# Performance work log

Measured on AMD Instinct MI355X. Metric: run time of the kernel, lower is better.

## Reference

```python
import jax, jax.numpy as jnp
import numpy as np

EPS = 1e-6
NQ, NKV, D, HID = 40, 8, 128, 5120
QKV_DIM = (NQ + 2 * NKV) * D + NQ  # gating enabled


def rmsnorm(x, w):
    xf = x.astype(jnp.float32)
    n = jax.lax.rsqrt(jnp.mean(xf * xf, axis=-1, keepdims=True) + EPS)
    return (xf * n).astype(x.dtype) * w


def rope(x, cos, sin):
    # x: [B,S,h,d], cos/sin: [B,S,d]
    d = x.shape[-1]
    c = cos[..., None, :d]
    s = sin[..., None, :d]
    x1, x2 = x[..., : d // 2], x[..., d // 2 :]
    rot = jnp.concatenate([-x2, x1], axis=-1)
    return x * c + rot * s


def setup_inputs() -> dict:
    key = jax.random.key(0)
    ks = jax.random.split(key, 8)
    B, S = 1, 2048
    return {
        "x": jax.random.normal(ks[0], (B, S, HID), jnp.float32),
        "rope_cos": jax.random.normal(ks[1], (B, S, D), jnp.float32),
        "rope_sin": jax.random.normal(ks[2], (B, S, D), jnp.float32),
        "w_pre_norm": jnp.ones((HID,), jnp.float32),
        "w_qkv": jax.random.normal(ks[3], (HID, QKV_DIM), jnp.float32) * 0.02,
        "w_q_norm": jnp.ones((D,), jnp.float32),
        "w_k_norm": jnp.ones((D,), jnp.float32),
        "w_proj": jax.random.normal(ks[4], (NQ * D, HID), jnp.float32) * 0.02,
    }


def reference(x, rope_cos, rope_sin, w_pre_norm, w_qkv, w_q_norm, w_k_norm, w_proj):
    B, S, _ = x.shape
    normed = rmsnorm(x, w_pre_norm)
    qkv = normed @ w_qkv  # [B,S,QKV_DIM]
    q_dim, k_dim = NQ * D, NKV * D
    q = qkv[..., :q_dim].reshape(B, S, NQ, D)
    k = qkv[..., q_dim : q_dim + k_dim].reshape(B, S, NKV, D)
    v = qkv[..., q_dim + k_dim : q_dim + 2 * k_dim].reshape(B, S, NKV, D)
    gate = jax.nn.sigmoid(qkv[..., q_dim + 2 * k_dim :])  # [B,S,NQ]
    q = rmsnorm(q, w_q_norm)
    k = rmsnorm(k, w_k_norm)
    q = rope(q, rope_cos, rope_sin)
    k = rope(k, rope_cos, rope_sin)
    # GQA: expand kv groups to query heads
    rep = NQ // NKV
    k = jnp.repeat(k, rep, axis=2)  # [B,S,NQ,D]
    v = jnp.repeat(v, rep, axis=2)
    scale = 1.0 / jnp.sqrt(jnp.float32(D))
    scores = jnp.einsum("bqhd,bkhd->bhqk", q, k) * scale
    attn = jax.nn.softmax(scores, axis=-1)
    out = jnp.einsum("bhqk,bkhd->bqhd", attn, v)  # [B,S,NQ,D]
    out = out * gate[..., None]
    out = out.reshape(B, S, NQ * D)
    return out @ w_proj
```

## Files before the change

kernel.cpp:

```cpp
#include <hip/hip_runtime.h>
#include <hip/hip_bf16.h>
#include <stdint.h>

#define S_LEN 2048
#define NQh   40
#define NKVh  8
#define HD    128
#define HIDd  5120
#define QKV_C 7208
#define QKV_P 7424
#define NROW  (S_LEN * NQh)

typedef unsigned short u16;
typedef short bf16x8 __attribute__((ext_vector_type(8)));
typedef float f32x4  __attribute__((ext_vector_type(4)));
typedef u16   u16x4  __attribute__((ext_vector_type(4)));

typedef const __attribute__((address_space(1))) void* gas_ptr;
typedef __attribute__((address_space(3))) void*       las_ptr;

#define MFMA16(a, b, c) __builtin_amdgcn_mfma_f32_16x16x32_bf16(a, b, c, 0, 0, 0)

__device__ __forceinline__ u16 f2bf(float f) {
  union { float f; unsigned u; } v; v.f = f;
  return (u16)((v.u + 0x7fffu + ((v.u >> 16) & 1u)) >> 16);
}
__device__ __forceinline__ u16 f2bf_c(float f) {
  union { __hip_bfloat16 b; u16 u; } v;
  v.b = __float2bfloat16(f);
  return v.u;
}
__device__ __forceinline__ float b2f(u16 b) {
  union { unsigned u; float f; } v; v.u = ((unsigned)b) << 16; return v.f;
}

__device__ __forceinline__ float wave_sum64(float x) {
#pragma unroll
  for (int m = 32; m > 0; m >>= 1) x += __shfl_xor(x, m, 64);
  return x;
}

__global__ __launch_bounds__(256) void prenorm_kernel(
    const float* __restrict__ x, const float* __restrict__ w, u16* __restrict__ xn) {
  int row = blockIdx.x;
  const float4* xr = (const float4*)(x + (size_t)row * HIDd);
  const float4* wr = (const float4*)w;
  float4 vx[5];
  float ss = 0.f;
#pragma unroll
  for (int c = 0; c < 5; ++c) {
    int i = c * 256 + threadIdx.x;
    vx[c] = xr[i];
    ss += vx[c].x * vx[c].x + vx[c].y * vx[c].y + vx[c].z * vx[c].z + vx[c].w * vx[c].w;
  }
  ss = wave_sum64(ss);
  __shared__ float red[4];
  if ((threadIdx.x & 63) == 0) red[threadIdx.x >> 6] = ss;
  __syncthreads();
  float tot = red[0] + red[1] + red[2] + red[3];
  float n = rsqrtf(tot * (1.f / HIDd) + 1e-6f);
  u16x4* out = (u16x4*)(xn + (size_t)row * HIDd);
#pragma unroll
  for (int c = 0; c < 5; ++c) {
    int i = c * 256 + threadIdx.x;
    float4 vw = wr[i];
    u16x4 o;
    o.x = f2bf(vx[c].x * n * vw.x);
    o.y = f2bf(vx[c].y * n * vw.y);
    o.z = f2bf(vx[c].z * n * vw.z);
    o.w = f2bf(vx[c].w * n * vw.w);
    out[i] = o;
  }
}

__global__ __launch_bounds__(256) void transpose_cvt(
    const float* __restrict__ src, u16* __restrict__ dst,
    int C, long ld_src, long ld_dst, long srcZ, long dstZ) {
  src += (long)blockIdx.z * srcZ;
  dst += (long)blockIdx.z * dstZ;
  __shared__ float t[32][33];
  int tx = threadIdx.x & 31, ty = threadIdx.x >> 5;
  int c0 = blockIdx.x * 32, r0 = blockIdx.y * 32;
#pragma unroll
  for (int i = 0; i < 32; i += 8) {
    int c = c0 + tx;
    t[ty + i][tx] = (c < C) ? src[(long)(r0 + ty + i) * ld_src + c] : 0.f;
  }
  __syncthreads();
#pragma unroll
  for (int i = 0; i < 32; i += 8) {
    int c = c0 + ty + i;
    dst[(long)c * ld_dst + (r0 + tx)] = f2bf(t[tx][ty + i]);
  }
}

__global__ __launch_bounds__(512, 1) void gemm8(
    const u16* __restrict__ A, const u16* __restrict__ BT, float* __restrict__ C,
    int M, int N, int K) {
  __shared__ __align__(16) char AL[65536];
  __shared__ __align__(16) char BL[65536];

  int tid = threadIdx.x, w = tid >> 6, l = tid & 63;
  int wm = w >> 2, wn = w & 3;
  int g = l >> 4, q = l & 15;

  int nwg = gridDim.x * gridDim.y;
  int wgid = blockIdx.y * gridDim.x + blockIdx.x;
  int cpx = nwg >> 3;
  int swz = (wgid & 7) * cpx + (wgid >> 3);
  int bx = swz % gridDim.x, by = swz / gridDim.x;
  long mBase = (long)by * 256, nBase = (long)bx * 256;
  long Kb = (long)K * 2;
  const char* Ag = (const char*)A + mBase * Kb;
  const char* Bg = (const char*)BT + nBase * Kb;

  int d0 = tid * 16, d1 = 8192 + tid * 16;
  long soff0 = (long)(d0 >> 6) * Kb + ((d0 & 63) ^ (((d0 >> 7) & 3) << 4));
  long soff1 = (long)(d1 >> 6) * Kb + ((d1 & 63) ^ (((d1 >> 7) & 3) << 4));

#define STG1(GBASE, LDSB, BUF, KH, T_)                                          \
  do {                                                                          \
    long kb_ = (long)(T_) * 128 + (KH) * 64;                                    \
    __builtin_amdgcn_global_load_lds((gas_ptr)((GBASE) + soff0 + kb_),          \
        (las_ptr)((LDSB) + (BUF) * 32768 + (KH) * 16384 + d0), 16, 0, 0);       \
    __builtin_amdgcn_global_load_lds((gas_ptr)((GBASE) + soff1 + kb_),          \
        (las_ptr)((LDSB) + (BUF) * 32768 + (KH) * 16384 + d1), 16, 0, 0);       \
  } while (0)

#define BARR                                                                    \
  do {                                                                          \
    __builtin_amdgcn_sched_barrier(0);                                          \
    __builtin_amdgcn_s_barrier();                                               \
    __builtin_amdgcn_sched_barrier(0);                                          \
  } while (0)
#define VMW(NLIT)                                                               \
  do {                                                                          \
    __builtin_amdgcn_sched_barrier(0);                                          \
    asm volatile("s_waitcnt vmcnt(" #NLIT ")" ::: "memory");                    \
    __builtin_amdgcn_sched_barrier(0);                                          \
  } while (0)

  int offA[8], offB[4];
#pragma unroll
  for (int i = 0; i < 8; ++i) {
    int r = wm * 128 + i * 16 + q;
    offA[i] = r * 64 + ((g * 16) ^ (((r >> 1) & 3) << 4));
  }
#pragma unroll
  for (int j = 0; j < 4; ++j) {
    int r = wn * 64 + j * 16 + q;
    offB[j] = r * 64 + ((g * 16) ^ (((r >> 1) & 3) << 4));
  }

#define PH_RDA(BASE, IG)                                                        \
  _Pragma("unroll") for (int ii = 0; ii < 4; ++ii)                              \
    af[ii] = *(const bf16x8*)((BASE) + offA[(IG) * 4 + ii]);
#define PH_RDB(BASE)                                                            \
  _Pragma("unroll") for (int j = 0; j < 4; ++j)                                 \
    bfr[j] = *(const bf16x8*)((BASE) + offB[j]);
#define PH_MFMA(IG)                                                             \
  do {                                                                          \
    __builtin_amdgcn_s_setprio(1);                                              \
    _Pragma("unroll") for (int ii = 0; ii < 4; ++ii)                            \
      _Pragma("unroll") for (int j = 0; j < 4; ++j)                             \
        acc[(IG) * 4 + ii][j] = MFMA16(af[ii], bfr[j], acc[(IG) * 4 + ii][j]);  \
    __builtin_amdgcn_s_setprio(0);                                              \
  } while (0)

  f32x4 acc[8][4] = {};
  int NT = K >> 6;

  STG1(Ag, AL, 0, 0, 0); STG1(Bg, BL, 0, 0, 0);
  STG1(Ag, AL, 0, 1, 0); STG1(Bg, BL, 0, 1, 0);
  STG1(Ag, AL, 1, 0, 1); STG1(Bg, BL, 1, 0, 1);
  VMW(8); BARR;

  for (int t = 0; t < NT; ++t) {
    int buf = t & 1, nb = buf ^ 1;
    const char* A0 = AL + buf * 32768;
    const char* B0 = BL + buf * 32768;
    const char* A1 = A0 + 16384;
    const char* B1 = B0 + 16384;
    bf16x8 af[4], bfr[4];

    PH_RDA(A0, 0); PH_RDB(B0);
    if (t + 1 < NT) STG1(Ag, AL, nb, 1, t + 1);
    BARR; PH_MFMA(0); BARR;
    PH_RDA(A0, 1);
    if (t + 1 < NT) { STG1(Bg, BL, nb, 1, t + 1); VMW(8); }
    else            { VMW(0); }
    BARR; PH_MFMA(1); BARR;
    PH_RDA(A1, 0); PH_RDB(B1);
    if (t + 2 < NT) STG1(Ag, AL, buf, 0, t + 2);
    BARR; PH_MFMA(0); BARR;
    PH_RDA(A1, 1);
    if (t + 2 < NT)      { STG1(Bg, BL, buf, 0, t + 2); VMW(8); }
    else if (t + 1 < NT) { VMW(4); }
    BARR; PH_MFMA(1); BARR;
  }
#undef STG1
#undef PH_RDA
#undef PH_RDB
#undef PH_MFMA
#undef BARR
#undef VMW

#pragma unroll
  for (int i = 0; i < 8; ++i)
#pragma unroll
    for (int j = 0; j < 4; ++j) {
      long mrow = mBase + wm * 128 + i * 16 + g * 4;
      long ncol = nBase + wn * 64 + j * 16 + q;
      float* cp = C + mrow * N + ncol;
#pragma unroll
      for (int r = 0; r < 4; ++r) cp[(long)r * N] = acc[i][j][r];
    }
}

__global__ __launch_bounds__(256) void split_kernel(
    const float* __restrict__ qkv, const float* __restrict__ cosb,
    const float* __restrict__ sinb, const float* __restrict__ wq,
    const float* __restrict__ wk, u16* __restrict__ qb, u16* __restrict__ kb,
    float* __restrict__ gate) {
  int s = blockIdx.x;
  int w = threadIdx.x >> 6, l = threadIdx.x & 63;
  const float* row = qkv + (size_t)s * QKV_P;
  float c0 = cosb[s * HD + l],      s0 = sinb[s * HD + l];
  float c1 = cosb[s * HD + 64 + l], s1 = sinb[s * HD + 64 + l];
  const float SCALE = 0.12751743f;
  for (int h = w; h < NQh; h += 4) {
    float x0 = row[h * HD + l], x1 = row[h * HD + 64 + l];
    float ss = wave_sum64(x0 * x0 + x1 * x1);
    float n = rsqrtf(ss * (1.f / HD) + 1e-6f);
    x0 *= n * wq[l]; x1 *= n * wq[64 + l];
    qb[((size_t)s * NQh + h) * HD + l]      = f2bf((x0 * c0 - x1 * s0) * SCALE);
    qb[((size_t)s * NQh + h) * HD + 64 + l] = f2bf((x1 * c1 + x0 * s1) * SCALE);
  }
  for (int h = w; h < NKVh; h += 4) {
    float x0 = row[NQh * HD + h * HD + l], x1 = row[NQh * HD + h * HD + 64 + l];
    float ss = wave_sum64(x0 * x0 + x1 * x1);
    float n = rsqrtf(ss * (1.f / HD) + 1e-6f);
    x0 *= n * wk[l]; x1 *= n * wk[64 + l];
    kb[((size_t)h * S_LEN + s) * HD + l]      = f2bf(x0 * c0 - x1 * s0);
    kb[((size_t)h * S_LEN + s) * HD + 64 + l] = f2bf(x1 * c1 + x0 * s1);
  }
  if (threadIdx.x < NQh) {
    float gx = row[(NQh + 2 * NKVh) * HD + threadIdx.x];
    gate[(size_t)s * NQh + threadIdx.x] = 1.f / (1.f + expf(-gx));
  }
}

__global__ __launch_bounds__(256) void attn_kernel(
    const u16* __restrict__ qb, const u16* __restrict__ kb,
    const u16* __restrict__ vT,
    u16* __restrict__ opart, float* __restrict__ lpart) {
  int L = blockIdx.x;
  int xcd = L & 7, t0 = L >> 3;
  int G = xcd * 10 + (t0 >> 4);
  int bx = t0 & 15;
  int h = G % NQh, z = G / NQh;
  int hk = h / 5;
  int w = threadIdx.x >> 6, l = threadIdx.x & 63;
  int g = l >> 4, q = l & 15;
  int s0 = bx * 128 + w * 32;
  int tid = threadIdx.x;

  __shared__ __align__(16) u16 Ks[2][32 * 128];
  __shared__ __align__(16) u16 Vs[2][128 * 32];
  __shared__ __align__(16) u16 Plds[4][2][16][40];

  bf16x8 ones;
#pragma unroll
  for (int j = 0; j < 8; ++j) ones[j] = (short)0x3F80;

  bf16x8 qf[2][4];
#pragma unroll
  for (int p = 0; p < 2; ++p)
#pragma unroll
    for (int kk = 0; kk < 4; ++kk)
      qf[p][kk] = *(const bf16x8*)(qb + ((size_t)(s0 + p * 16 + q) * NQh + h) * HD + kk * 32 + g * 8);

  const char* KhB = (const char*)(kb + ((size_t)hk * S_LEN + z * 1024) * HD);
  const char* VhB = (const char*)(vT + (size_t)hk * HD * S_LEN + z * 1024);

  int Dk0 = tid * 16, Dk1 = 4096 + tid * 16;
  long ks0 = (long)(Dk0 >> 8) * 256 + ((Dk0 & 255) ^ (((Dk0 >> 8) & 7) << 4));
  long ks1 = (long)(Dk1 >> 8) * 256 + ((Dk1 & 255) ^ (((Dk1 >> 8) & 7) << 4));
  long vs0 = (long)(Dk0 >> 6) * 4096 + ((Dk0 & 63) ^ (((Dk0 >> 7) & 3) << 4));
  long vs1 = (long)(Dk1 >> 6) * 4096 + ((Dk1 & 63) ^ (((Dk1 >> 7) & 3) << 4));

#define STG(BUF, T_)                                                            \
  do {                                                                          \
    __builtin_amdgcn_global_load_lds((gas_ptr)(KhB + (long)(T_) * 8192 + ks0),  \
        (las_ptr)((char*)&Ks[BUF][0] + Dk0), 16, 0, 0);                         \
    __builtin_amdgcn_global_load_lds((gas_ptr)(KhB + (long)(T_) * 8192 + ks1),  \
        (las_ptr)((char*)&Ks[BUF][0] + Dk1), 16, 0, 0);                         \
    __builtin_amdgcn_global_load_lds((gas_ptr)(VhB + (long)(T_) * 64 + vs0),    \
        (las_ptr)((char*)&Vs[BUF][0] + Dk0), 16, 0, 0);                         \
    __builtin_amdgcn_global_load_lds((gas_ptr)(VhB + (long)(T_) * 64 + vs1),    \
        (las_ptr)((char*)&Vs[BUF][0] + Dk1), 16, 0, 0);                         \
  } while (0)

#define BARR                                                                    \
  do {                                                                          \
    __builtin_amdgcn_sched_barrier(0);                                          \
    __builtin_amdgcn_s_barrier();                                               \
    __builtin_amdgcn_sched_barrier(0);                                          \
  } while (0)

  f32x4 oacc[8][2] = {};
  f32x4 lacc[2] = {};
  int xq = (q & 7) << 4;
  int xv = ((q >> 1) & 3) << 4;

  STG(0, 0); STG(1, 1);
  __builtin_amdgcn_sched_barrier(0);
  asm volatile("s_waitcnt vmcnt(4)" ::: "memory");
  BARR;

  for (int step = 0; step < 32; ++step) {
    const char* kc = (const char*)&Ks[step & 1][0];
    const char* vc = (const char*)&Vs[step & 1][0];

    f32x4 sacc[2][2] = {};
#pragma unroll
    for (int kk = 0; kk < 4; ++kk) {
#pragma unroll
      for (int kt = 0; kt < 2; ++kt) {
        bf16x8 kf = *(const bf16x8*)(kc + (kt * 16 + q) * 256 + ((kk * 64 + g * 16) ^ xq));
        sacc[kt][0] = MFMA16(kf, qf[0][kk], sacc[kt][0]);
        sacc[kt][1] = MFMA16(kf, qf[1][kk], sacc[kt][1]);
      }
    }
    bf16x8 va[8];
#pragma unroll
    for (int dt = 0; dt < 8; ++dt)
      va[dt] = *(const bf16x8*)(vc + (dt * 16 + q) * 64 + ((g * 16) ^ xv));

#pragma unroll
    for (int p = 0; p < 2; ++p) {
#pragma unroll
      for (int kt = 0; kt < 2; ++kt) {
        u16x4 pk;
#pragma unroll
        for (int r = 0; r < 4; ++r) pk[r] = f2bf_c(exp2f(sacc[kt][p][r]));
        *(u16x4*)&Plds[w][p][q][kt * 16 + g * 4] = pk;
      }
    }
    bf16x8 pf0 = *(const bf16x8*)&Plds[w][0][q][g * 8];
    bf16x8 pf1 = *(const bf16x8*)&Plds[w][1][q][g * 8];
    __builtin_amdgcn_s_setprio(1);
#pragma unroll
    for (int dt = 0; dt < 8; ++dt) {
      oacc[dt][0] = MFMA16(va[dt], pf0, oacc[dt][0]);
      oacc[dt][1] = MFMA16(va[dt], pf1, oacc[dt][1]);
    }
    lacc[0] = MFMA16(ones, pf0, lacc[0]);
    lacc[1] = MFMA16(ones, pf1, lacc[1]);
    __builtin_amdgcn_s_setprio(0);

    BARR;
    if (step + 2 < 32) {
      STG(step & 1, step + 2);
      __builtin_amdgcn_sched_barrier(0);
      asm volatile("s_waitcnt vmcnt(4)" ::: "memory");
      __builtin_amdgcn_sched_barrier(0);
    } else if (step + 1 < 32) {
      __builtin_amdgcn_sched_barrier(0);
      asm volatile("s_waitcnt vmcnt(0)" ::: "memory");
      __builtin_amdgcn_sched_barrier(0);
    }
    BARR;
  }
#undef STG
#undef BARR

#pragma unroll
  for (int p = 0; p < 2; ++p) {
    size_t row = (size_t)(s0 + p * 16 + q) * NQh + h;
    if (g == 0) lpart[(size_t)z * NROW + row] = lacc[p][0];
    u16* op = opart + ((size_t)z * NROW + row) * HD;
#pragma unroll
    for (int dt = 0; dt < 8; ++dt) {
      u16x4 o;
#pragma unroll
      for (int r = 0; r < 4; ++r) o[r] = f2bf_c(oacc[dt][p][r]);
      *(u16x4*)(op + dt * 16 + g * 4) = o;
    }
  }
}

__global__ __launch_bounds__(256) void combine_kernel(
    const u16* __restrict__ opart, const float* __restrict__ lpart,
    const float* __restrict__ gate, u16* __restrict__ ob) {
  int t = blockIdx.x * 256 + threadIdx.x;
  int row = t >> 5, dv = (t & 31) * 4;
  float l0 = lpart[row], l1 = lpart[NROW + row];
  float sc = gate[row] / (l0 + l1);
  u16x4 o0 = *(const u16x4*)(opart + (size_t)row * HD + dv);
  u16x4 o1 = *(const u16x4*)(opart + (size_t)NROW * HD + (size_t)row * HD + dv);
  u16x4 o;
#pragma unroll
  for (int r = 0; r < 4; ++r) o[r] = f2bf(sc * (b2f(o0[r]) + b2f(o1[r])));
  *(u16x4*)(ob + (size_t)row * HD + dv) = o;
}

extern "C" void kernel_launch(void* const* d_in, const int* in_sizes, int n_in,
                              void* d_out, int out_size, void* d_ws, size_t ws_size,
                              hipStream_t stream) {
  const float* x     = (const float*)d_in[0];
  const float* rc    = (const float*)d_in[1];
  const float* rs    = (const float*)d_in[2];
  const float* wpre  = (const float*)d_in[3];
  const float* wqkv  = (const float*)d_in[4];
  const float* wqn   = (const float*)d_in[5];
  const float* wkn   = (const float*)d_in[6];
  const float* wproj = (const float*)d_in[7];
  float* out = (float*)d_out;

  char* ws = (char*)d_ws;
  size_t off = 0;
  auto alloc = [&](size_t bytes) -> void* {
    void* p = ws + off;
    off += (bytes + 255) & ~(size_t)255;
    return p;
  };
  u16*   xn     = (u16*)  alloc((size_t)S_LEN * HIDd * 2);
  u16*   wqkvT  = (u16*)  alloc((size_t)QKV_P * HIDd * 2);
  u16*   wprojT = (u16*)  alloc((size_t)HIDd * HIDd * 2);
  float* qkv    = (float*)alloc((size_t)S_LEN * QKV_P * 4);
  u16*   qb     = (u16*)  alloc((size_t)S_LEN * NQh * HD * 2);
  u16*   kb     = (u16*)  alloc((size_t)NKVh * S_LEN * HD * 2);
  u16*   vT     = (u16*)  alloc((size_t)NKVh * HD * S_LEN * 2);
  float* gate   = (float*)alloc((size_t)S_LEN * NQh * 4);
  u16*   ob     = (u16*)  alloc((size_t)S_LEN * NQh * HD * 2);
  if (off > ws_size) return;

  u16*   opart = (u16*)ws;
  float* lpart = (float*)(opart + (size_t)2 * NROW * HD);

  prenorm_kernel<<<S_LEN, 256, 0, stream>>>(x, wpre, xn);
  transpose_cvt<<<dim3(QKV_P / 32, HIDd / 32, 1), 256, 0, stream>>>(
      wqkv, wqkvT, QKV_C, (long)QKV_C, (long)HIDd, 0, 0);
  transpose_cvt<<<dim3(HIDd / 32, HIDd / 32, 1), 256, 0, stream>>>(
      wproj, wprojT, HIDd, (long)HIDd, (long)HIDd, 0, 0);
  gemm8<<<dim3(QKV_P / 256, S_LEN / 256), 512, 0, stream>>>(
      xn, wqkvT, qkv, S_LEN, QKV_P, HIDd);
  split_kernel<<<S_LEN, 256, 0, stream>>>(qkv, rc, rs, wqn, wkn, qb, kb, gate);
  transpose_cvt<<<dim3(HD / 32, S_LEN / 32, NKVh), 256, 0, stream>>>(
      qkv + (NQh + NKVh) * HD, vT, HD, (long)QKV_P, (long)S_LEN,
      128, (long)HD * S_LEN);
  attn_kernel<<<1280, 256, 0, stream>>>(qb, kb, vT, opart, lpart);
  combine_kernel<<<NROW * 32 / 256, 256, 0, stream>>>(
      opart, lpart, gate, ob);
  gemm8<<<dim3(HIDd / 256, S_LEN / 256), 512, 0, stream>>>(
      ob, wprojT, out, S_LEN, HIDd, HIDd);
}
```

Baseline: 640.7 us.

## Merge GEMM half-phases into 32-MFMA blocks and vectorize transpose

The GEMM main loop goes from four phases of 16 MFMAs, each with its own barrier pair, to two phases of 32 MFMAs. Each phase reads all 8 A fragments and 4 B fragments at once and issues both A and B global-to-LDS stages together. This halves the barrier count per K-tile but raises register use and changes how LDS reads overlap with MFMAs. Some sched_barriers are dropped to give the compiler more freedom. The transpose_cvt kernel now uses float2 loads and 4-wide bf16 stores to cut the number of memory transactions.

```diff
diff --git a/kernel.cpp b/kernel.cpp
--- a/kernel.cpp
+++ b/kernel.cpp
@@ -78,19 +78,30 @@
     int C, long ld_src, long ld_dst, long srcZ, long dstZ) {
   src += (long)blockIdx.z * srcZ;
   dst += (long)blockIdx.z * dstZ;
-  __shared__ float t[32][33];
-  int tx = threadIdx.x & 31, ty = threadIdx.x >> 5;
+  __shared__ float t[32][34];
   int c0 = blockIdx.x * 32, r0 = blockIdx.y * 32;
-#pragma unroll
-  for (int i = 0; i < 32; i += 8) {
-    int c = c0 + tx;
-    t[ty + i][tx] = (c < C) ? src[(long)(r0 + ty + i) * ld_src + c] : 0.f;
+  {
+    int lc = threadIdx.x & 15, lr = threadIdx.x >> 4;
+#pragma unroll
+    for (int i = 0; i < 32; i += 16) {
+      int r = r0 + lr + i;
+      int c = c0 + lc * 2;
+      float2 v = make_float2(0.f, 0.f);
+      if (c < C) v = *(const float2*)(src + (long)r * ld_src + c);
+      *(float2*)&t[lr + i][lc * 2] = v;
+    }
   }
   __syncthreads();
-#pragma unroll
-  for (int i = 0; i < 32; i += 8) {
-    int c = c0 + ty + i;
-    dst[(long)c * ld_dst + (r0 + tx)] = f2bf(t[tx][ty + i]);
+  {
+    int cc = threadIdx.x >> 3;
+    int rq = (threadIdx.x & 7) * 4;
+    int c = c0 + cc;
+    if (c < C) {
+      u16x4 o;
+#pragma unroll
+      for (int rr = 0; rr < 4; ++rr) o[rr] = f2bf(t[rq + rr][cc]);
+      *(u16x4*)(dst + (long)c * ld_dst + (r0 + rq)) = o;
+    }
   }
 }
 
@@ -129,13 +140,11 @@
 
 #define BARR                                                                    \
   do {                                                                          \
-    __builtin_amdgcn_sched_barrier(0);                                          \
     __builtin_amdgcn_s_barrier();                                               \
     __builtin_amdgcn_sched_barrier(0);                                          \
   } while (0)
 #define VMW(NLIT)                                                               \
   do {                                                                          \
-    __builtin_amdgcn_sched_barrier(0);                                          \
     asm volatile("s_waitcnt vmcnt(" #NLIT ")" ::: "memory");                    \
     __builtin_amdgcn_sched_barrier(0);                                          \
   } while (0)
@@ -152,18 +161,19 @@
     offB[j] = r * 64 + ((g * 16) ^ (((r >> 1) & 3) << 4));
   }
 
-#define PH_RDA(BASE, IG)                                                        \
-  _Pragma("unroll") for (int ii = 0; ii < 4; ++ii)                              \
-    af[ii] = *(const bf16x8*)((BASE) + offA[(IG) * 4 + ii]);
-#define PH_RDB(BASE)                                                            \
-  _Pragma("unroll") for (int j = 0; j < 4; ++j)                                 \
-    bfr[j] = *(const bf16x8*)((BASE) + offB[j]);
-#define PH_MFMA(IG)                                                             \
+#define RD_ALL(ABASE, BBASE)                                                    \
+  do {                                                                          \
+    _Pragma("unroll") for (int ii = 0; ii < 8; ++ii)                            \
+      af[ii] = *(const bf16x8*)((ABASE) + offA[ii]);                            \
+    _Pragma("unroll") for (int j = 0; j < 4; ++j)                               \
+      bfr[j] = *(const bf16x8*)((BBASE) + offB[j]);                             \
+  } while (0)
+#define MFMA32                                                                  \
   do {                                                                          \
     __builtin_amdgcn_s_setprio(1);                                              \
-    _Pragma("unroll") for (int ii = 0; ii < 4; ++ii)                            \
+    _Pragma("unroll") for (int ii = 0; ii < 8; ++ii)                            \
       _Pragma("unroll") for (int j = 0; j < 4; ++j)                             \
-        acc[(IG) * 4 + ii][j] = MFMA16(af[ii], bfr[j], acc[(IG) * 4 + ii][j]);  \
+        acc[ii][j] = MFMA16(af[ii], bfr[j], acc[ii][j]);                        \
     __builtin_amdgcn_s_setprio(0);                                              \
   } while (0)
 
@@ -177,31 +187,27 @@
 
   for (int t = 0; t < NT; ++t) {
     int buf = t & 1, nb = buf ^ 1;
-    const char* A0 = AL + buf * 32768;
-    const char* B0 = BL + buf * 32768;
-    const char* A1 = A0 + 16384;
-    const char* B1 = B0 + 16384;
-    bf16x8 af[4], bfr[4];
-
-    PH_RDA(A0, 0); PH_RDB(B0);
-    if (t + 1 < NT) STG1(Ag, AL, nb, 1, t + 1);
-    BARR; PH_MFMA(0); BARR;
-    PH_RDA(A0, 1);
-    if (t + 1 < NT) { STG1(Bg, BL, nb, 1, t + 1); VMW(8); }
+    const char* Abuf = AL + buf * 32768;
+    const char* Bbuf = BL + buf * 32768;
+    bf16x8 af[8], bfr[4];
+
+    RD_ALL(Abuf, Bbuf);
+    if (t + 1 < NT) { STG1(Ag, AL, nb, 1, t + 1); STG1(Bg, BL, nb, 1, t + 1); VMW(8); }
     else            { VMW(0); }
-    BARR; PH_MFMA(1); BARR;
-    PH_RDA(A1, 0); PH_RDB(B1);
-    if (t + 2 < NT) STG1(Ag, AL, buf, 0, t + 2);
-    BARR; PH_MFMA(0); BARR;
-    PH_RDA(A1, 1);
-    if (t + 2 < NT)      { STG1(Bg, BL, buf, 0, t + 2); VMW(8); }
+    BARR;
+    MFMA32;
+    BARR;
+
+    RD_ALL(Abuf + 16384, Bbuf + 16384);
+    if (t + 2 < NT)      { STG1(Ag, AL, buf, 0, t + 2); STG1(Bg, BL, buf, 0, t + 2); VMW(8); }
     else if (t + 1 < NT) { VMW(4); }
-    BARR; PH_MFMA(1); BARR;
+    BARR;
+    MFMA32;
+    BARR;
   }
 #undef STG1
-#undef PH_RDA
-#undef PH_RDB
-#undef PH_MFMA
+#undef RD_ALL
+#undef MFMA32
 #undef BARR
 #undef VMW
 
```

Result: faster. 622.7 us (-2.8%).
